# Kernel optimization log

Hardware: AMD Instinct MI355X
Metric: run time of the kernel (lower is better)

## Reference

```python
import jax, jax.numpy as jnp
import numpy as np

NEG_INF = -1e9

def setup_inputs() -> dict:
    key = jax.random.key(0)
    kq, kk, kv, kt, km = jax.random.split(key, 5)
    B, H, S, D = 2, 16, 2048, 64
    query = jax.random.normal(kq, (B, H, S, D), dtype=jnp.float32)
    k_ = jax.random.normal(kk, (B, H, S, D), dtype=jnp.float32)
    value = jax.random.normal(kv, (B, H, S, D), dtype=jnp.float32)
    time = jax.random.normal(kt, (B, H, S, D), dtype=jnp.float32)
    mask = jax.random.randint(km, (B, 1, S, S), 0, 2, dtype=jnp.int32)
    return {"query": query, "key": k_, "value": value, "time": time, "mask": mask}

def reference(query, key, value, time, mask):
    # scores = (Q K^T + Q T^T) / sqrt(D)  == Q (K+T)^T / sqrt(D)
    scale = 1.0 / jnp.sqrt(jnp.asarray(query.shape[-1], query.dtype))
    query_time = jnp.einsum('bhqd,bhkd->bhqk', query, time) * scale
    query_key = jnp.einsum('bhqd,bhkd->bhqk', query, key) * scale
    scores = query_time + query_key
    scores = jnp.where(mask == 0, jnp.asarray(NEG_INF, scores.dtype), scores)
    p_attn = jax.nn.softmax(scores, axis=-1)
    out = jnp.einsum('bhqk,bhkd->bhqd', p_attn, value)
    return (out, p_attn)
```

## Files before the change

kernel.cpp:

```cpp
#include <hip/hip_runtime.h>
#include <hip/hip_bf16.h>

#define TA_B 2
#define TA_H 16
#define TA_S 2048
#define TA_D 64
#define KTILE 64
#define QB 128
#define BLOCK 512
#define NKT (TA_S / KTILE)

typedef __attribute__((ext_vector_type(4))) float f32x4;
typedef __attribute__((ext_vector_type(8))) short bf16x8;
typedef __attribute__((ext_vector_type(8))) unsigned short u16x8;
typedef __attribute__((ext_vector_type(4))) unsigned short u16x4;
typedef __attribute__((ext_vector_type(2))) unsigned int u32x2;

union BF8 { u16x8 u; bf16x8 s; };

__device__ __forceinline__ unsigned short f2bf(float f) {
    union { float f; unsigned int i; } v; v.f = f;
    unsigned int x = v.i;
    unsigned int r = x + 0x7FFFu + ((x >> 16) & 1u);
    return (unsigned short)(r >> 16);
}
__device__ __forceinline__ float bf2f(unsigned short u) {
    union { unsigned int i; float f; } v; v.i = ((unsigned int)u) << 16; return v.f;
}

__device__ __forceinline__ void barrier_lds() {
    asm volatile("s_waitcnt lgkmcnt(0)" ::: "memory");
    __builtin_amdgcn_sched_barrier(0);
    __builtin_amdgcn_s_barrier();
    __builtin_amdgcn_sched_barrier(0);
}

__global__ __launch_bounds__(256) void pack_mask(const int* __restrict__ M,
                                                 unsigned long long* __restrict__ Mp) {
    const int nw = TA_B * TA_S * NKT;
    const int wavesTotal = (gridDim.x * blockDim.x) >> 6;
    const int wid  = (blockIdx.x * blockDim.x + threadIdx.x) >> 6;
    const int lane = threadIdx.x & 63;
    for (int w = wid; w < nw; w += wavesTotal) {
        int mv = M[(long)w * 64 + lane];
        unsigned long long bits = __ballot(mv != 0);
        if (lane == 0) Mp[w] = bits;
    }
}

template <bool PACKED>
__global__ __launch_bounds__(BLOCK, 4) void ta_fused(
    const float* __restrict__ Qg,
    const float* __restrict__ Kg,
    const float* __restrict__ Vg,
    const float* __restrict__ Tg,
    const int* __restrict__ Mg,
    const unsigned long long* __restrict__ Mp,
    float* __restrict__ Og,
    float* __restrict__ Pg)
{
    __shared__ unsigned short sKp[2][KTILE][72];
    __shared__ unsigned short sVt[2][TA_D][72];
    __shared__ unsigned short sP[QB][72];

    const int tid  = threadIdx.x;
    const int wave = tid >> 6;
    const int lane = tid & 63;
    const int c    = lane & 15;
    const int g    = lane >> 4;
    const int row0 = tid >> 3;
    const int cg   = (tid & 7) * 8;

    const int did = blockIdx.x + 16 * (blockIdx.y + 16 * blockIdx.z);
    const int wid = (did & 7) * 64 + (did >> 3);
    const int q0  = (wid & 15) * QB;
    const int h   = (wid >> 4) & 15;
    const int b   = wid >> 8;

    const long bh    = (long)b * TA_H + h;
    const long xBase = bh * (long)TA_S * TA_D;
    const long pBase = bh * (long)TA_S * TA_S;
    const long mBase = (long)b * (long)TA_S * TA_S;
    const int  wq0   = wave * 16;
    const int  myq   = q0 + wq0 + c;

    bf16x8 qf0, qf1;
    {
        const float* qp = Qg + xBase + (long)myq * TA_D + g * 8;
        f32x4 a0 = *(const f32x4*)(qp);
        f32x4 a1 = *(const f32x4*)(qp + 4);
        f32x4 b0 = *(const f32x4*)(qp + 32);
        f32x4 b1 = *(const f32x4*)(qp + 36);
        BF8 u0, u1;
#pragma unroll
        for (int i = 0; i < 4; ++i) {
            u0.u[i]     = f2bf(a0[i] * 0.125f);
            u0.u[i + 4] = f2bf(a1[i] * 0.125f);
            u1.u[i]     = f2bf(b0[i] * 0.125f);
            u1.u[i + 4] = f2bf(b1[i] * 0.125f);
        }
        qf0 = u0.s; qf1 = u1.s;
    }

    f32x4 kA0, kA1, tA0, tA1, vA0, vA1;

    auto loadKT = [&](int kt) {
        const long o0 = xBase + (long)(kt * KTILE + row0) * TA_D + cg;
        kA0 = *(const f32x4*)(Kg + o0); kA1 = *(const f32x4*)(Kg + o0 + 4);
        tA0 = *(const f32x4*)(Tg + o0); tA1 = *(const f32x4*)(Tg + o0 + 4);
    };
    auto loadV = [&](int kt) {
        const long o0 = xBase + (long)(kt * KTILE + row0) * TA_D + cg;
        vA0 = *(const f32x4*)(Vg + o0); vA1 = *(const f32x4*)(Vg + o0 + 4);
    };
    auto storeKp = [&](int p) {
        u16x8 r0;
#pragma unroll
        for (int i = 0; i < 4; ++i) {
            r0[i]     = f2bf(kA0[i] + tA0[i]);
            r0[i + 4] = f2bf(kA1[i] + tA1[i]);
        }
        *(u16x8*)&sKp[p][row0][cg] = r0;
    };
    auto storeVt = [&](int p) {
        const int kp = row0 ^ cg;
#pragma unroll
        for (int i = 0; i < 4; ++i) {
            sVt[p][cg + i][kp]     = f2bf(vA0[i]);
            sVt[p][cg + i + 4][kp] = f2bf(vA1[i]);
        }
    };

    auto maskWord = [&](int kt) -> unsigned long long {
        if constexpr (PACKED) {
            return Mp[((long)b * TA_S + myq) * NKT + kt];
        } else {
            const int* mp = Mg + mBase + (long)myq * TA_S + kt * KTILE;
            unsigned long long w = 0;
#pragma unroll
            for (int ct = 0; ct < 4; ++ct)
#pragma unroll
                for (int r = 0; r < 4; ++r)
                    w |= mp[ct * 16 + g * 4 + r] ? (1ull << (ct * 16 + g * 4 + r)) : 0ull;
            return w;
        }
    };

    float lpart = 0.0f;
    loadKT(0);
    for (int kt = 0; kt < NKT; ++kt) {
        const int p = kt & 1;
        storeKp(p);
        loadKT(kt + 1 < NKT ? kt + 1 : 0);
        barrier_lds();

        f32x4 acc[4];
#pragma unroll
        for (int ct = 0; ct < 4; ++ct)
#pragma unroll
            for (int j = 0; j < 4; ++j) acc[ct][j] = 0.0f;

        __builtin_amdgcn_s_setprio(1);
#pragma unroll
        for (int kk = 0; kk < 2; ++kk) {
            bf16x8 qa = kk ? qf1 : qf0;
#pragma unroll
            for (int ct = 0; ct < 4; ++ct) {
                BF8 bf; bf.u = *(const u16x8*)&sKp[p][ct * 16 + c][kk * 32 + g * 8];
                acc[ct] = __builtin_amdgcn_mfma_f32_16x16x32_bf16(bf.s, qa, acc[ct], 0, 0, 0);
            }
        }
        __builtin_amdgcn_s_setprio(0);

        const unsigned long long w = maskWord(kt);
#pragma unroll
        for (int ct = 0; ct < 4; ++ct) {
            const unsigned nib = (unsigned)(w >> (ct * 16 + g * 4)) & 0xFu;
#pragma unroll
            for (int r = 0; r < 4; ++r)
                lpart += ((nib >> r) & 1u) ? __expf(acc[ct][r]) : 0.0f;
        }
    }

    loadV(0);

    float l = lpart;
    l += __shfl_xor(l, 16);
    l += __shfl_xor(l, 32);
    const float invl = (l > 0.0f) ? (1.0f / l) : 0.0f;

    f32x4 oacc[4];
#pragma unroll
    for (int dt = 0; dt < 4; ++dt)
#pragma unroll
        for (int j = 0; j < 4; ++j) oacc[dt][j] = 0.0f;

    for (int kt = 0; kt < NKT; ++kt) {
        const int p = kt & 1;
        storeKp(p);
        storeVt(p);
        const int ktn = kt + 1 < NKT ? kt + 1 : 0;
        loadKT(ktn);
        loadV(ktn);
        barrier_lds();

        f32x4 acc[4];
#pragma unroll
        for (int ct = 0; ct < 4; ++ct)
#pragma unroll
            for (int j = 0; j < 4; ++j) acc[ct][j] = 0.0f;

        __builtin_amdgcn_s_setprio(1);
#pragma unroll
        for (int kk = 0; kk < 2; ++kk) {
            bf16x8 qa = kk ? qf1 : qf0;
#pragma unroll
            for (int ct = 0; ct < 4; ++ct) {
                BF8 bf; bf.u = *(const u16x8*)&sKp[p][ct * 16 + c][kk * 32 + g * 8];
                acc[ct] = __builtin_amdgcn_mfma_f32_16x16x32_bf16(bf.s, qa, acc[ct], 0, 0, 0);
            }
        }
        __builtin_amdgcn_s_setprio(0);

        const unsigned long long w = maskWord(kt);
#pragma unroll
        for (int ct = 0; ct < 4; ++ct) {
            const unsigned nib = (unsigned)(w >> (ct * 16 + g * 4)) & 0xFu;
            float pv[4];
#pragma unroll
            for (int r = 0; r < 4; ++r) {
                float e = ((nib >> r) & 1u) ? __expf(acc[ct][r]) : 0.0f;
                pv[r] = e * invl;
            }
            u32x2 pk;
            pk[0] = (unsigned)f2bf(pv[0]) | ((unsigned)f2bf(pv[1]) << 16);
            pk[1] = (unsigned)f2bf(pv[2]) | ((unsigned)f2bf(pv[3]) << 16);
            *(u32x2*)&sP[wq0 + c][ct * 16 + g * 4] = pk;
        }

        BF8 pa0, pa1;
        pa0.u = *(const u16x8*)&sP[wq0 + c][g * 8];
        pa1.u = *(const u16x8*)&sP[wq0 + c][32 + g * 8];
        __builtin_amdgcn_s_setprio(1);
#pragma unroll
        for (int dt = 0; dt < 4; ++dt) {
            const int dRow = dt * 16 + c;
            const int kc0 = (g * 8) ^ (dRow & 56);
            const int kc1 = (32 + g * 8) ^ (dRow & 56);
            BF8 bv0, bv1;
            bv0.u = *(const u16x8*)&sVt[p][dRow][kc0];
            oacc[dt] = __builtin_amdgcn_mfma_f32_16x16x32_bf16(pa0.s, bv0.s, oacc[dt], 0, 0, 0);
            bv1.u = *(const u16x8*)&sVt[p][dRow][kc1];
            oacc[dt] = __builtin_amdgcn_mfma_f32_16x16x32_bf16(pa1.s, bv1.s, oacc[dt], 0, 0, 0);
        }
        __builtin_amdgcn_s_setprio(0);

#pragma unroll
        for (int j = 0; j < 4; ++j) {
            const int prow = 4 * j + g;
            u16x4 pv = *(const u16x4*)&sP[wq0 + prow][c * 4];
            f32x4 v;
#pragma unroll
            for (int i = 0; i < 4; ++i) v[i] = bf2f(pv[i]);
            __builtin_nontemporal_store(
                v, (f32x4*)(Pg + pBase + (long)(q0 + wq0 + prow) * TA_S + kt * KTILE + c * 4));
        }
    }

#pragma unroll
    for (int dt = 0; dt < 4; ++dt) {
#pragma unroll
        for (int r = 0; r < 4; ++r) {
            __builtin_nontemporal_store(
                oacc[dt][r],
                &Og[xBase + (long)(q0 + wq0 + g * 4 + r) * TA_D + dt * 16 + c]);
        }
    }
}

extern "C" void kernel_launch(void* const* d_in, const int* in_sizes, int n_in,
                              void* d_out, int out_size, void* d_ws, size_t ws_size,
                              hipStream_t stream) {
    const float* Q = (const float*)d_in[0];
    const float* K = (const float*)d_in[1];
    const float* V = (const float*)d_in[2];
    const float* T = (const float*)d_in[3];
    const int*   M = (const int*)d_in[4];

    float* O = (float*)d_out;
    float* P = O + (long)TA_B * TA_H * TA_S * TA_D;

    unsigned long long* Mp = (unsigned long long*)d_ws;
    const size_t needWs = (size_t)TA_B * TA_S * NKT * sizeof(unsigned long long);

    dim3 grid(TA_S / QB, TA_H, TA_B);
    dim3 block(BLOCK);

    if (ws_size >= needWs) {
        hipLaunchKernelGGL(pack_mask, dim3(512), dim3(256), 0, stream, M, Mp);
        hipLaunchKernelGGL(ta_fused<true>, grid, block, 0, stream, Q, K, V, T, M, Mp, O, P);
    } else {
        hipLaunchKernelGGL(ta_fused<false>, grid, block, 0, stream, Q, K, V, T, M, Mp, O, P);
    }
}
```

Before: 193.1 us.

## Single-buffer K/V shared tiles with extra barriers to raise occupancy

```diff
diff --git a/kernel.cpp b/kernel.cpp
--- a/kernel.cpp
+++ b/kernel.cpp
@@ -49,7 +49,7 @@
 }
 
 template <bool PACKED>
-__global__ __launch_bounds__(BLOCK, 4) void ta_fused(
+__global__ __launch_bounds__(BLOCK, 6) void ta_fused(
     const float* __restrict__ Qg,
     const float* __restrict__ Kg,
     const float* __restrict__ Vg,
@@ -59,8 +59,8 @@
     float* __restrict__ Og,
     float* __restrict__ Pg)
 {
-    __shared__ unsigned short sKp[2][KTILE][72];
-    __shared__ unsigned short sVt[2][TA_D][72];
+    __shared__ unsigned short sKp[KTILE][72];
+    __shared__ unsigned short sVt[TA_D][72];
     __shared__ unsigned short sP[QB][72];
 
     const int tid  = threadIdx.x;
@@ -113,21 +113,21 @@
         const long o0 = xBase + (long)(kt * KTILE + row0) * TA_D + cg;
         vA0 = *(const f32x4*)(Vg + o0); vA1 = *(const f32x4*)(Vg + o0 + 4);
     };
-    auto storeKp = [&](int p) {
+    auto storeKp = [&]() {
         u16x8 r0;
 #pragma unroll
         for (int i = 0; i < 4; ++i) {
             r0[i]     = f2bf(kA0[i] + tA0[i]);
             r0[i + 4] = f2bf(kA1[i] + tA1[i]);
         }
-        *(u16x8*)&sKp[p][row0][cg] = r0;
-    };
-    auto storeVt = [&](int p) {
+        *(u16x8*)&sKp[row0][cg] = r0;
+    };
+    auto storeVt = [&]() {
         const int kp = row0 ^ cg;
 #pragma unroll
         for (int i = 0; i < 4; ++i) {
-            sVt[p][cg + i][kp]     = f2bf(vA0[i]);
-            sVt[p][cg + i + 4][kp] = f2bf(vA1[i]);
+            sVt[cg + i][kp]     = f2bf(vA0[i]);
+            sVt[cg + i + 4][kp] = f2bf(vA1[i]);
         }
     };
 
@@ -149,8 +149,7 @@
     float lpart = 0.0f;
     loadKT(0);
     for (int kt = 0; kt < NKT; ++kt) {
-        const int p = kt & 1;
-        storeKp(p);
+        storeKp();
         loadKT(kt + 1 < NKT ? kt + 1 : 0);
         barrier_lds();
 
@@ -166,11 +165,12 @@
             bf16x8 qa = kk ? qf1 : qf0;
 #pragma unroll
             for (int ct = 0; ct < 4; ++ct) {
-                BF8 bf; bf.u = *(const u16x8*)&sKp[p][ct * 16 + c][kk * 32 + g * 8];
+                BF8 bf; bf.u = *(const u16x8*)&sKp[ct * 16 + c][kk * 32 + g * 8];
                 acc[ct] = __builtin_amdgcn_mfma_f32_16x16x32_bf16(bf.s, qa, acc[ct], 0, 0, 0);
             }
         }
         __builtin_amdgcn_s_setprio(0);
+        barrier_lds();
 
         const unsigned long long w = maskWord(kt);
 #pragma unroll
@@ -196,9 +196,8 @@
         for (int j = 0; j < 4; ++j) oacc[dt][j] = 0.0f;
 
     for (int kt = 0; kt < NKT; ++kt) {
-        const int p = kt & 1;
-        storeKp(p);
-        storeVt(p);
+        storeKp();
+        storeVt();
         const int ktn = kt + 1 < NKT ? kt + 1 : 0;
         loadKT(ktn);
         loadV(ktn);
@@ -216,7 +215,7 @@
             bf16x8 qa = kk ? qf1 : qf0;
 #pragma unroll
             for (int ct = 0; ct < 4; ++ct) {
-                BF8 bf; bf.u = *(const u16x8*)&sKp[p][ct * 16 + c][kk * 32 + g * 8];
+                BF8 bf; bf.u = *(const u16x8*)&sKp[ct * 16 + c][kk * 32 + g * 8];
                 acc[ct] = __builtin_amdgcn_mfma_f32_16x16x32_bf16(bf.s, qa, acc[ct], 0, 0, 0);
             }
         }
@@ -248,12 +247,13 @@
             const int kc0 = (g * 8) ^ (dRow & 56);
             const int kc1 = (32 + g * 8) ^ (dRow & 56);
             BF8 bv0, bv1;
-            bv0.u = *(const u16x8*)&sVt[p][dRow][kc0];
+            bv0.u = *(const u16x8*)&sVt[dRow][kc0];
             oacc[dt] = __builtin_amdgcn_mfma_f32_16x16x32_bf16(pa0.s, bv0.s, oacc[dt], 0, 0, 0);
-            bv1.u = *(const u16x8*)&sVt[p][dRow][kc1];
+            bv1.u = *(const u16x8*)&sVt[dRow][kc1];
             oacc[dt] = __builtin_amdgcn_mfma_f32_16x16x32_bf16(pa1.s, bv1.s, oacc[dt], 0, 0, 0);
         }
         __builtin_amdgcn_s_setprio(0);
+        barrier_lds();
 
 #pragma unroll
         for (int j = 0; j < 4; ++j) {
```

Result: slower. 378.7 us (+96.1%).

## Split softmax denominator pass into separate split-K kernel for more parallelism

Applied to the files above, without the earlier changes.

```diff
diff --git a/kernel.cpp b/kernel.cpp
--- a/kernel.cpp
+++ b/kernel.cpp
@@ -9,6 +9,8 @@
 #define QB 128
 #define BLOCK 512
 #define NKT (TA_S / KTILE)
+#define NSPLIT 4
+#define KT_PER (NKT / NSPLIT)
 
 typedef __attribute__((ext_vector_type(4))) float f32x4;
 typedef __attribute__((ext_vector_type(8))) short bf16x8;
@@ -48,20 +50,14 @@
     }
 }
 
-template <bool PACKED>
-__global__ __launch_bounds__(BLOCK, 4) void ta_fused(
+__global__ __launch_bounds__(BLOCK, 4) void ta_passA(
     const float* __restrict__ Qg,
     const float* __restrict__ Kg,
-    const float* __restrict__ Vg,
     const float* __restrict__ Tg,
-    const int* __restrict__ Mg,
     const unsigned long long* __restrict__ Mp,
-    float* __restrict__ Og,
-    float* __restrict__ Pg)
+    float* __restrict__ wsL)
 {
     __shared__ unsigned short sKp[2][KTILE][72];
-    __shared__ unsigned short sVt[2][TA_D][72];
-    __shared__ unsigned short sP[QB][72];
 
     const int tid  = threadIdx.x;
     const int wave = tid >> 6;
@@ -71,18 +67,18 @@
     const int row0 = tid >> 3;
     const int cg   = (tid & 7) * 8;
 
-    const int did = blockIdx.x + 16 * (blockIdx.y + 16 * blockIdx.z);
-    const int wid = (did & 7) * 64 + (did >> 3);
-    const int q0  = (wid & 15) * QB;
-    const int h   = (wid >> 4) & 15;
-    const int b   = wid >> 8;
+    const int did = blockIdx.x + 64 * (blockIdx.y + 16 * blockIdx.z);
+    const int wid = (did & 7) * 256 + (did >> 3);
+    const int q0    = (wid & 15) * QB;
+    const int split = (wid >> 4) & 3;
+    const int h     = (wid >> 6) & 15;
+    const int b     = wid >> 10;
 
     const long bh    = (long)b * TA_H + h;
     const long xBase = bh * (long)TA_S * TA_D;
-    const long pBase = bh * (long)TA_S * TA_S;
-    const long mBase = (long)b * (long)TA_S * TA_S;
     const int  wq0   = wave * 16;
     const int  myq   = q0 + wq0 + c;
+    const int  kt0   = split * KT_PER;
 
     bf16x8 qf0, qf1;
     {
@@ -102,17 +98,12 @@
         qf0 = u0.s; qf1 = u1.s;
     }
 
-    f32x4 kA0, kA1, tA0, tA1, vA0, vA1;
-
+    f32x4 kA0, kA1, tA0, tA1;
     auto loadKT = [&](int kt) {
         const long o0 = xBase + (long)(kt * KTILE + row0) * TA_D + cg;
         kA0 = *(const f32x4*)(Kg + o0); kA1 = *(const f32x4*)(Kg + o0 + 4);
         tA0 = *(const f32x4*)(Tg + o0); tA1 = *(const f32x4*)(Tg + o0 + 4);
     };
-    auto loadV = [&](int kt) {
-        const long o0 = xBase + (long)(kt * KTILE + row0) * TA_D + cg;
-        vA0 = *(const f32x4*)(Vg + o0); vA1 = *(const f32x4*)(Vg + o0 + 4);
-    };
     auto storeKp = [&](int p) {
         u16x8 r0;
 #pragma unroll
@@ -122,36 +113,14 @@
         }
         *(u16x8*)&sKp[p][row0][cg] = r0;
     };
-    auto storeVt = [&](int p) {
-        const int kp = row0 ^ cg;
-#pragma unroll
-        for (int i = 0; i < 4; ++i) {
-            sVt[p][cg + i][kp]     = f2bf(vA0[i]);
-            sVt[p][cg + i + 4][kp] = f2bf(vA1[i]);
-        }
-    };
-
-    auto maskWord = [&](int kt) -> unsigned long long {
-        if constexpr (PACKED) {
-            return Mp[((long)b * TA_S + myq) * NKT + kt];
-        } else {
-            const int* mp = Mg + mBase + (long)myq * TA_S + kt * KTILE;
-            unsigned long long w = 0;
-#pragma unroll
-            for (int ct = 0; ct < 4; ++ct)
-#pragma unroll
-                for (int r = 0; r < 4; ++r)
-                    w |= mp[ct * 16 + g * 4 + r] ? (1ull << (ct * 16 + g * 4 + r)) : 0ull;
-            return w;
-        }
-    };
 
     float lpart = 0.0f;
-    loadKT(0);
-    for (int kt = 0; kt < NKT; ++kt) {
-        const int p = kt & 1;
+    loadKT(kt0);
+    for (int i = 0; i < KT_PER; ++i) {
+        const int kt = kt0 + i;
+        const int p  = i & 1;
         storeKp(p);
-        loadKT(kt + 1 < NKT ? kt + 1 : 0);
+        loadKT(i + 1 < KT_PER ? kt + 1 : kt0);
         barrier_lds();
 
         f32x4 acc[4];
@@ -172,7 +141,7 @@
         }
         __builtin_amdgcn_s_setprio(0);
 
-        const unsigned long long w = maskWord(kt);
+        const unsigned long long w = Mp[((long)b * TA_S + myq) * NKT + kt];
 #pragma unroll
         for (int ct = 0; ct < 4; ++ct) {
             const unsigned nib = (unsigned)(w >> (ct * 16 + g * 4)) & 0xFu;
@@ -181,13 +150,100 @@
                 lpart += ((nib >> r) & 1u) ? __expf(acc[ct][r]) : 0.0f;
         }
     }
-
-    loadV(0);
 
     float l = lpart;
     l += __shfl_xor(l, 16);
     l += __shfl_xor(l, 32);
-    const float invl = (l > 0.0f) ? (1.0f / l) : 0.0f;
+    if (g == 0)
+        wsL[((long)bh * TA_S + myq) * NSPLIT + split] = l;
+}
+
+__global__ __launch_bounds__(BLOCK, 4) void ta_passB(
+    const float* __restrict__ Qg,
+    const float* __restrict__ Kg,
+    const float* __restrict__ Vg,
+    const float* __restrict__ Tg,
+    const unsigned long long* __restrict__ Mp,
+    const float* __restrict__ wsL,
+    float* __restrict__ Og,
+    float* __restrict__ Pg)
+{
+    __shared__ unsigned short sKp[2][KTILE][72];
+    __shared__ unsigned short sVt[2][TA_D][72];
+    __shared__ unsigned short sP[QB][72];
+
+    const int tid  = threadIdx.x;
+    const int wave = tid >> 6;
+    const int lane = tid & 63;
+    const int c    = lane & 15;
+    const int g    = lane >> 4;
+    const int row0 = tid >> 3;
+    const int cg   = (tid & 7) * 8;
+
+    const int did = blockIdx.x + 16 * (blockIdx.y + 16 * blockIdx.z);
+    const int wid = (did & 7) * 64 + (did >> 3);
+    const int q0  = (wid & 15) * QB;
+    const int h   = (wid >> 4) & 15;
+    const int b   = wid >> 8;
+
+    const long bh    = (long)b * TA_H + h;
+    const long xBase = bh * (long)TA_S * TA_D;
+    const long pBase = bh * (long)TA_S * TA_S;
+    const int  wq0   = wave * 16;
+    const int  myq   = q0 + wq0 + c;
+
+    bf16x8 qf0, qf1;
+    {
+        const float* qp = Qg + xBase + (long)myq * TA_D + g * 8;
+        f32x4 a0 = *(const f32x4*)(qp);
+        f32x4 a1 = *(const f32x4*)(qp + 4);
+        f32x4 b0 = *(const f32x4*)(qp + 32);
+        f32x4 b1 = *(const f32x4*)(qp + 36);
+        BF8 u0, u1;
+#pragma unroll
+        for (int i = 0; i < 4; ++i) {
+            u0.u[i]     = f2bf(a0[i] * 0.125f);
+            u0.u[i + 4] = f2bf(a1[i] * 0.125f);
+            u1.u[i]     = f2bf(b0[i] * 0.125f);
+            u1.u[i + 4] = f2bf(b1[i] * 0.125f);
+        }
+        qf0 = u0.s; qf1 = u1.s;
+    }
+
+    float invl;
+    {
+        f32x4 lp = *(const f32x4*)&wsL[((long)bh * TA_S + myq) * NSPLIT];
+        float l = lp[0] + lp[1] + lp[2] + lp[3];
+        invl = (l > 0.0f) ? (1.0f / l) : 0.0f;
+    }
+
+    f32x4 kA0, kA1, tA0, tA1, vA0, vA1;
+    auto loadKT = [&](int kt) {
+        const long o0 = xBase + (long)(kt * KTILE + row0) * TA_D + cg;
+        kA0 = *(const f32x4*)(Kg + o0); kA1 = *(const f32x4*)(Kg + o0 + 4);
+        tA0 = *(const f32x4*)(Tg + o0); tA1 = *(const f32x4*)(Tg + o0 + 4);
+    };
+    auto loadV = [&](int kt) {
+        const long o0 = xBase + (long)(kt * KTILE + row0) * TA_D + cg;
+        vA0 = *(const f32x4*)(Vg + o0); vA1 = *(const f32x4*)(Vg + o0 + 4);
+    };
+    auto storeKp = [&](int p) {
+        u16x8 r0;
+#pragma unroll
+        for (int i = 0; i < 4; ++i) {
+            r0[i]     = f2bf(kA0[i] + tA0[i]);
+            r0[i + 4] = f2bf(kA1[i] + tA1[i]);
+        }
+        *(u16x8*)&sKp[p][row0][cg] = r0;
+    };
+    auto storeVt = [&](int p) {
+        const int kp = row0 ^ cg;
+#pragma unroll
+        for (int i = 0; i < 4; ++i) {
+            sVt[p][cg + i][kp]     = f2bf(vA0[i]);
+            sVt[p][cg + i + 4][kp] = f2bf(vA1[i]);
+        }
+    };
 
     f32x4 oacc[4];
 #pragma unroll
@@ -195,6 +251,8 @@
 #pragma unroll
         for (int j = 0; j < 4; ++j) oacc[dt][j] = 0.0f;
 
+    loadKT(0);
+    loadV(0);
     for (int kt = 0; kt < NKT; ++kt) {
         const int p = kt & 1;
         storeKp(p);
@@ -222,7 +280,7 @@
         }
         __builtin_amdgcn_s_setprio(0);
 
-        const unsigned long long w = maskWord(kt);
+        const unsigned long long w = Mp[((long)b * TA_S + myq) * NKT + kt];
 #pragma unroll
         for (int ct = 0; ct < 4; ++ct) {
             const unsigned nib = (unsigned)(w >> (ct * 16 + g * 4)) & 0xFu;
@@ -278,6 +336,221 @@
     }
 }
 
+__global__ __launch_bounds__(BLOCK, 4) void ta_mono(
+    const float* __restrict__ Qg,
+    const float* __restrict__ Kg,
+    const float* __restrict__ Vg,
+    const float* __restrict__ Tg,
+    const int* __restrict__ Mg,
+    float* __restrict__ Og,
+    float* __restrict__ Pg)
+{
+    __shared__ unsigned short sKp[2][KTILE][72];
+    __shared__ unsigned short sVt[2][TA_D][72];
+    __shared__ unsigned short sP[QB][72];
+
+    const int tid  = threadIdx.x;
+    const int wave = tid >> 6;
+    const int lane = tid & 63;
+    const int c    = lane & 15;
+    const int g    = lane >> 4;
+    const int row0 = tid >> 3;
+    const int cg   = (tid & 7) * 8;
+
+    const int did = blockIdx.x + 16 * (blockIdx.y + 16 * blockIdx.z);
+    const int wid = (did & 7) * 64 + (did >> 3);
+    const int q0  = (wid & 15) * QB;
+    const int h   = (wid >> 4) & 15;
+    const int b   = wid >> 8;
+
+    const long bh    = (long)b * TA_H + h;
+    const long xBase = bh * (long)TA_S * TA_D;
+    const long pBase = bh * (long)TA_S * TA_S;
+    const long mBase = (long)b * (long)TA_S * TA_S;
+    const int  wq0   = wave * 16;
+    const int  myq   = q0 + wq0 + c;
+
+    bf16x8 qf0, qf1;
+    {
+        const float* qp = Qg + xBase + (long)myq * TA_D + g * 8;
+        f32x4 a0 = *(const f32x4*)(qp);
+        f32x4 a1 = *(const f32x4*)(qp + 4);
+        f32x4 b0 = *(const f32x4*)(qp + 32);
+        f32x4 b1 = *(const f32x4*)(qp + 36);
+        BF8 u0, u1;
+#pragma unroll
+        for (int i = 0; i < 4; ++i) {
+            u0.u[i]     = f2bf(a0[i] * 0.125f);
+            u0.u[i + 4] = f2bf(a1[i] * 0.125f);
+            u1.u[i]     = f2bf(b0[i] * 0.125f);
+            u1.u[i + 4] = f2bf(b1[i] * 0.125f);
+        }
+        qf0 = u0.s; qf1 = u1.s;
+    }
+
+    f32x4 kA0, kA1, tA0, tA1, vA0, vA1;
+    auto loadKT = [&](int kt) {
+        const long o0 = xBase + (long)(kt * KTILE + row0) * TA_D + cg;
+        kA0 = *(const f32x4*)(Kg + o0); kA1 = *(const f32x4*)(Kg + o0 + 4);
+        tA0 = *(const f32x4*)(Tg + o0); tA1 = *(const f32x4*)(Tg + o0 + 4);
+    };
+    auto loadV = [&](int kt) {
+        const long o0 = xBase + (long)(kt * KTILE + row0) * TA_D + cg;
+        vA0 = *(const f32x4*)(Vg + o0); vA1 = *(const f32x4*)(Vg + o0 + 4);
+    };
+    auto storeKp = [&](int p) {
+        u16x8 r0;
+#pragma unroll
+        for (int i = 0; i < 4; ++i) {
+            r0[i]     = f2bf(kA0[i] + tA0[i]);
+            r0[i + 4] = f2bf(kA1[i] + tA1[i]);
+        }
+        *(u16x8*)&sKp[p][row0][cg] = r0;
+    };
+    auto storeVt = [&](int p) {
+        const int kp = row0 ^ cg;
+#pragma unroll
+        for (int i = 0; i < 4; ++i) {
+            sVt[p][cg + i][kp]     = f2bf(vA0[i]);
+            sVt[p][cg + i + 4][kp] = f2bf(vA1[i]);
+        }
+    };
+    auto maskWord = [&](int kt) -> unsigned long long {
+        const int* mp = Mg + mBase + (long)myq * TA_S + kt * KTILE;
+        unsigned long long w = 0;
+#pragma unroll
+        for (int ct = 0; ct < 4; ++ct)
+#pragma unroll
+            for (int r = 0; r < 4; ++r)
+                w |= mp[ct * 16 + g * 4 + r] ? (1ull << (ct * 16 + g * 4 + r)) : 0ull;
+        return w;
+    };
+
+    float lpart = 0.0f;
+    loadKT(0);
+    for (int kt = 0; kt < NKT; ++kt) {
+        const int p = kt & 1;
+        storeKp(p);
+        loadKT(kt + 1 < NKT ? kt + 1 : 0);
+        barrier_lds();
+
+        f32x4 acc[4];
+#pragma unroll
+        for (int ct = 0; ct < 4; ++ct)
+#pragma unroll
+            for (int j = 0; j < 4; ++j) acc[ct][j] = 0.0f;
+
+#pragma unroll
+        for (int kk = 0; kk < 2; ++kk) {
+            bf16x8 qa = kk ? qf1 : qf0;
+#pragma unroll
+            for (int ct = 0; ct < 4; ++ct) {
+                BF8 bf; bf.u = *(const u16x8*)&sKp[p][ct * 16 + c][kk * 32 + g * 8];
+                acc[ct] = __builtin_amdgcn_mfma_f32_16x16x32_bf16(bf.s, qa, acc[ct], 0, 0, 0);
+            }
+        }
+
+        const unsigned long long w = maskWord(kt);
+#pragma unroll
+        for (int ct = 0; ct < 4; ++ct) {
+            const unsigned nib = (unsigned)(w >> (ct * 16 + g * 4)) & 0xFu;
+#pragma unroll
+            for (int r = 0; r < 4; ++r)
+                lpart += ((nib >> r) & 1u) ? __expf(acc[ct][r]) : 0.0f;
+        }
+    }
+
+    loadV(0);
+    float l = lpart;
+    l += __shfl_xor(l, 16);
+    l += __shfl_xor(l, 32);
+    const float invl = (l > 0.0f) ? (1.0f / l) : 0.0f;
+
+    f32x4 oacc[4];
+#pragma unroll
+    for (int dt = 0; dt < 4; ++dt)
+#pragma unroll
+        for (int j = 0; j < 4; ++j) oacc[dt][j] = 0.0f;
+
+    for (int kt = 0; kt < NKT; ++kt) {
+        const int p = kt & 1;
+        storeKp(p);
+        storeVt(p);
+        const int ktn = kt + 1 < NKT ? kt + 1 : 0;
+        loadKT(ktn);
+        loadV(ktn);
+        barrier_lds();
+
+        f32x4 acc[4];
+#pragma unroll
+        for (int ct = 0; ct < 4; ++ct)
+#pragma unroll
+            for (int j = 0; j < 4; ++j) acc[ct][j] = 0.0f;
+
+#pragma unroll
+        for (int kk = 0; kk < 2; ++kk) {
+            bf16x8 qa = kk ? qf1 : qf0;
+#pragma unroll
+            for (int ct = 0; ct < 4; ++ct) {
+                BF8 bf; bf.u = *(const u16x8*)&sKp[p][ct * 16 + c][kk * 32 + g * 8];
+                acc[ct] = __builtin_amdgcn_mfma_f32_16x16x32_bf16(bf.s, qa, acc[ct], 0, 0, 0);
+            }
+        }
+
+        const unsigned long long w = maskWord(kt);
+#pragma unroll
+        for (int ct = 0; ct < 4; ++ct) {
+            const unsigned nib = (unsigned)(w >> (ct * 16 + g * 4)) & 0xFu;
+            float pv[4];
+#pragma unroll
+            for (int r = 0; r < 4; ++r) {
+                float e = ((nib >> r) & 1u) ? __expf(acc[ct][r]) : 0.0f;
+                pv[r] = e * invl;
+            }
+            u32x2 pk;
+            pk[0] = (unsigned)f2bf(pv[0]) | ((unsigned)f2bf(pv[1]) << 16);
+            pk[1] = (unsigned)f2bf(pv[2]) | ((unsigned)f2bf(pv[3]) << 16);
+            *(u32x2*)&sP[wq0 + c][ct * 16 + g * 4] = pk;
+        }
+
+        BF8 pa0, pa1;
+        pa0.u = *(const u16x8*)&sP[wq0 + c][g * 8];
+        pa1.u = *(const u16x8*)&sP[wq0 + c][32 + g * 8];
+#pragma unroll
+        for (int dt = 0; dt < 4; ++dt) {
+            const int dRow = dt * 16 + c;
+            const int kc0 = (g * 8) ^ (dRow & 56);
+            const int kc1 = (32 + g * 8) ^ (dRow & 56);
+            BF8 bv0, bv1;
+            bv0.u = *(const u16x8*)&sVt[p][dRow][kc0];
+            oacc[dt] = __builtin_amdgcn_mfma_f32_16x16x32_bf16(pa0.s, bv0.s, oacc[dt], 0, 0, 0);
+            bv1.u = *(const u16x8*)&sVt[p][dRow][kc1];
+            oacc[dt] = __builtin_amdgcn_mfma_f32_16x16x32_bf16(pa1.s, bv1.s, oacc[dt], 0, 0, 0);
+        }
+
+#pragma unroll
+        for (int j = 0; j < 4; ++j) {
+            const int prow = 4 * j + g;
+            u16x4 pv = *(const u16x4*)&sP[wq0 + prow][c * 4];
+            f32x4 v;
+#pragma unroll
+            for (int i = 0; i < 4; ++i) v[i] = bf2f(pv[i]);
+            __builtin_nontemporal_store(
+                v, (f32x4*)(Pg + pBase + (long)(q0 + wq0 + prow) * TA_S + kt * KTILE + c * 4));
+        }
+    }
+
+#pragma unroll
+    for (int dt = 0; dt < 4; ++dt) {
+#pragma unroll
+        for (int r = 0; r < 4; ++r) {
+            __builtin_nontemporal_store(
+                oacc[dt][r],
+                &Og[xBase + (long)(q0 + wq0 + g * 4 + r) * TA_D + dt * 16 + c]);
+        }
+    }
+}
+
 extern "C" void kernel_launch(void* const* d_in, const int* in_sizes, int n_in,
                               void* d_out, int out_size, void* d_ws, size_t ws_size,
                               hipStream_t stream) {
@@ -290,16 +563,19 @@
     float* O = (float*)d_out;
     float* P = O + (long)TA_B * TA_H * TA_S * TA_D;
 
+    const size_t maskWs = (size_t)TA_B * TA_S * NKT * 8;
+    const size_t lWs    = (size_t)TA_B * TA_H * TA_S * NSPLIT * 4;
+
     unsigned long long* Mp = (unsigned long long*)d_ws;
-    const size_t needWs = (size_t)TA_B * TA_S * NKT * sizeof(unsigned long long);
-
-    dim3 grid(TA_S / QB, TA_H, TA_B);
+    float* wsL = (float*)((char*)d_ws + maskWs);
+
     dim3 block(BLOCK);
 
-    if (ws_size >= needWs) {
+    if (ws_size >= maskWs + lWs) {
         hipLaunchKernelGGL(pack_mask, dim3(512), dim3(256), 0, stream, M, Mp);
-        hipLaunchKernelGGL(ta_fused<true>, grid, block, 0, stream, Q, K, V, T, M, Mp, O, P);
+        hipLaunchKernelGGL(ta_passA, dim3(64, 16, 2), block, 0, stream, Q, K, T, Mp, wsL);
+        hipLaunchKernelGGL(ta_passB, dim3(16, 16, 2), block, 0, stream, Q, K, V, T, Mp, wsL, O, P);
     } else {
-        hipLaunchKernelGGL(ta_fused<false>, grid, block, 0, stream, Q, K, V, T, M, Mp, O, P);
-    }
-}
+        hipLaunchKernelGGL(ta_mono, dim3(16, 16, 2), block, 0, stream, Q, K, V, T, M, O, P);
+    }
+}
```

New measurement: 193.3 us (median of 2 runs). No clear change (+0.1%).
